# Optimization experiments

Measured on AMD Instinct MI355X. Metric: run time of the kernel, lower is better.

## Reference

```python
import jax, jax.numpy as jnp
import numpy as np
from jax import lax


def _conv3d(x, w, b, circular=False):
    # x: (B,C,D,H,W), w: (O,I,kd,kh,kw)
    if circular:
        x = jnp.pad(x, ((0, 0), (0, 0), (1, 1), (1, 1), (1, 1)), mode='wrap')
    y = lax.conv_general_dilated(x, w, (1, 1, 1), 'VALID',
                                 dimension_numbers=('NCDHW', 'OIDHW', 'NCDHW'))
    return y + b[None, :, None, None, None]


def _inorm(x):
    # InstanceNorm3d, affine=False, eps=1e-5, biased variance over spatial dims
    mu = jnp.mean(x, axis=(2, 3, 4), keepdims=True)
    var = jnp.var(x, axis=(2, 3, 4), keepdims=True)
    return (x - mu) * lax.rsqrt(var + 1e-5)


def _gelu(x):
    return jax.nn.gelu(x, approximate=False)


def _r6_to_matrix(r6):
    eps = 1e-7
    v1 = r6[..., :3]
    v1 = v1 / (jnp.linalg.norm(v1, axis=-1, keepdims=True) + eps)
    v2 = r6[..., 3:]
    v2 = v2 - jnp.sum(v2 * v1, -1, keepdims=True) * v1
    v2 = v2 / (jnp.linalg.norm(v2, axis=-1, keepdims=True) + eps)
    v3 = jnp.cross(v1, v2)
    det = jnp.linalg.det(jnp.stack([v1, v2, v3], axis=-2))
    v3 = jnp.where(det[..., None] < 0, -v3, v3)
    return jnp.stack([v1, v2, v3], axis=-2)


def _ensure_matrix(R):
    def fnorm(v):
        return v / jnp.maximum(jnp.linalg.norm(v, axis=-1, keepdims=True), 1e-12)
    v1 = fnorm(R[..., 0, :] + 1e-6)
    v2 = R[..., 1, :]
    v2 = fnorm(v2 - jnp.sum(v2 * v1, -1, keepdims=True) * v1 + 1e-6)
    v3 = jnp.cross(v1, v2)
    det = jnp.linalg.det(jnp.stack([v1, v2, v3], axis=-2))
    v3 = jnp.where(det[..., None] < 0, -v3, v3)
    Rn = jnp.stack([v1, v2, v3], axis=-2)
    Rt = jnp.swapaxes(Rn, -2, -1)
    return 0.5 * (Rn + Rt @ Rn @ Rt)


def _rotate(X, R):
    # X: (bd, nh, L, hd); R: (nh, 3, 3). Pads hd to a multiple of 3, rotates
    # each 3-vector group by R^T-on-the-right (X_rot = X @ R^T).
    hd = X.shape[-1]
    pad = (-hd) % 3
    Xp = jnp.pad(X, ((0, 0), (0, 0), (0, 0), (0, pad))) if pad else X
    nv = Xp.shape[-1] // 3
    Xr = Xp.reshape(Xp.shape[:-1] + (nv, 3))
    Y = jnp.einsum('bhlvi,hji->bhlvj', Xr, R).reshape(Xp.shape)
    return Y[..., :hd] if pad else Y


def _forward(x, pos_emb, qkv_w, qkv_b, lp_w1, lp_b1, lp_w2, lp_b2,
             mod_w1, mod_b1, mod_w2, mod_b2, pa_w, pa_b,
             proj_w, proj_b, pos_bias_w, pos_bias_b,
             A_d, A_h, A_w, R_d, R_h, R_w, t_d, t_h, t_w):
    B, C, D, H, W = x.shape
    nh = pa_w.shape[0]
    hd = C // nh
    scale = hd ** -0.5

    # PositionalProcessing (identical for all three axial passes)
    lf = _conv3d(pos_emb, lp_w1, lp_b1, circular=True)
    lf = _conv3d(_gelu(_inorm(lf)), lp_w2, lp_b2)
    m = _conv3d(lf, mod_w1, mod_b1)
    m = jax.nn.sigmoid(_conv3d(_gelu(_inorm(m)), mod_w2, mod_b2))
    x_mod = x * m                                   # (B,C,D,H,W)
    pa = _gelu(_inorm(_conv3d(pos_emb, pa_w, pa_b)))  # (B,nh,D,H,W)

    def axial(comp, perm, inv_perm, A, R, t):
        xp = jnp.transpose(x_mod, perm)             # (B, a, b, C, L)
        Bp, a, b, _, L = xp.shape
        bd = Bp * a * b
        xf = jnp.swapaxes(xp.reshape(bd, C, L), 1, 2)  # (bd, L, C)
        qkv = (xf @ qkv_w.T + qkv_b).reshape(bd, L, 3, nh, hd)
        qkv = jnp.transpose(qkv, (2, 0, 3, 1, 4))
        q, k, v = qkv[0], qkv[1], qkv[2]
        R_qk = _r6_to_matrix(A[0].astype(jnp.float32))  # (nh,3,3), same for all bd
        R_v = _ensure_matrix(R[0])                      # (nh,3,3)
        q_r, k_r, v_r = _rotate(q, R_qk), _rotate(k, R_qk), _rotate(v, R_v)
        # axis positions: linspace on one coordinate component
        pos = jnp.zeros((L, 3), x.dtype).at[:, comp].set(jnp.linspace(-1.0, 1.0, L))
        pos_t = pos[None] + t[0]                        # (nh, L, 3)
        rel = pos_t[:, :, None, :] - pos_t[:, None, :, :]  # (nh, L, L, 3)
        bias = jnp.einsum('hqkc,c->hqk', rel, pos_bias_w[0]) + pos_bias_b[0]
        pa_p = jnp.transpose(pa, perm).reshape(bd, nh, L)
        attn = jnp.einsum('bhqd,bhkd->bhqk', q_r, k_r) * scale
        attn = jax.nn.softmax(attn + pa_p[..., None] + bias[None], axis=-1)
        out = jnp.einsum('bhqk,bhkd->bhqd', attn, v_r)
        out = jnp.transpose(out, (0, 2, 1, 3)).reshape(Bp, a, b, L, C)
        return jnp.transpose(out, inv_perm)             # back to (B,C,D,H,W)

    out = (axial(2, (0, 3, 4, 1, 2), (0, 4, 3, 1, 2), A_d, R_d, t_d)
           + axial(1, (0, 2, 4, 1, 3), (0, 4, 1, 3, 2), A_h, R_h, t_h)
           + axial(0, (0, 2, 3, 1, 4), (0, 4, 1, 2, 3), A_w, R_w, t_w))
    return jnp.einsum('oc,bcdhw->bodhw', proj_w[:, :, 0, 0, 0], out) + proj_b[None, :, None, None, None]


def setup_inputs() -> dict:
    key = jax.random.key(0)
    B, C, D, H, W, nh = 2, 128, 32, 32, 32, 8
    ks = jax.random.split(key, 24)

    def n(k, shape, s=0.05):
        return (jax.random.normal(k, shape) * s).astype(jnp.float32)

    def r6(k):
        k1, k2 = jax.random.split(k)
        v1 = jax.random.normal(k1, (1, nh, 3))
        v1 = v1 / jnp.linalg.norm(v1, axis=-1, keepdims=True)
        v2 = jax.random.normal(k2, (1, nh, 3))
        v2 = v2 - jnp.sum(v2 * v1, -1, keepdims=True) * v1
        v2 = v2 / jnp.linalg.norm(v2, axis=-1, keepdims=True)
        return jnp.concatenate([v1, v2], -1).astype(jnp.float32)

    eye = jnp.broadcast_to(jnp.eye(3, dtype=jnp.float32), (1, nh, 3, 3))
    return {
        'x': jax.random.normal(ks[0], (B, C, D, H, W), jnp.float32),
        'pos_emb': jax.random.normal(ks[1], (B, C, D, H, W), jnp.float32),
        'qkv_w': n(ks[2], (3 * C, C)), 'qkv_b': n(ks[3], (3 * C,)),
        'lp_w1': n(ks[4], (C, C, 3, 3, 3), 0.02), 'lp_b1': n(ks[5], (C,)),
        'lp_w2': n(ks[6], (C, C, 1, 1, 1)), 'lp_b2': n(ks[7], (C,)),
        'mod_w1': n(ks[8], (C, C, 1, 1, 1)), 'mod_b1': n(ks[9], (C,)),
        'mod_w2': n(ks[10], (C, C, 1, 1, 1)), 'mod_b2': n(ks[11], (C,)),
        'pa_w': n(ks[12], (nh, C, 1, 1, 1)), 'pa_b': n(ks[13], (nh,)),
        'proj_w': n(ks[14], (C, C, 1, 1, 1)), 'proj_b': n(ks[15], (C,)),
        'pos_bias_w': n(ks[16], (1, 3), 0.5), 'pos_bias_b': n(ks[17], (1,)),
        'A_d': r6(ks[18]), 'A_h': r6(ks[19]), 'A_w': r6(ks[20]),
        'R_d': eye, 'R_h': eye, 'R_w': eye,
        't_d': n(ks[21], (1, nh, 1, 3), 0.01),
        't_h': n(ks[22], (1, nh, 1, 3), 0.01),
        't_w': n(ks[23], (1, nh, 1, 3), 0.01),
    }


def reference(x, pos_emb, qkv_w, qkv_b, lp_w1, lp_b1, lp_w2, lp_b2,
              mod_w1, mod_b1, mod_w2, mod_b2, pa_w, pa_b,
              proj_w, proj_b, pos_bias_w, pos_bias_b,
              A_d, A_h, A_w, R_d, R_h, R_w, t_d, t_h, t_w):
    return _forward(x, pos_emb, qkv_w, qkv_b, lp_w1, lp_b1, lp_w2, lp_b2,
                    mod_w1, mod_b1, mod_w2, mod_b2, pa_w, pa_b,
                    proj_w, proj_b, pos_bias_w, pos_bias_b,
                    A_d, A_h, A_w, R_d, R_h, R_w, t_d, t_h, t_w)
```

## Files before the change

### kernel.cpp

```cpp
#include <hip/hip_runtime.h>
#include <cstdint>
#include <cstddef>


#define NTOK 65536
#define SPAT 32768

#define WS_R0     0ull
#define WS_A0     0ull
#define WS_A1     4194304ull
#define WS_MPREB  8388608ull
#define WS_A2     8388608ull
#define WS_XTOKB  12582912ull
#define WS_INT    16777216ull
#define WS_QKVH   20971520ull
#define WS_CONVP  33554432ull
#define WS_QKVP   33775616ull
#define WS_WCP    33800192ull
#define WS_MODW2P 33808384ull
#define WS_PROJP  33816576ull
#define WS_BC     33824768ull
#define WS_RBUF   33824896ull
#define WS_PS     33825328ull
#define WS_PSS    33956400ull
#define WS_MU1    34087472ull
#define WS_RS1    34087728ull
#define WS_MU2    34087984ull
#define WS_RS2    34088240ull

typedef __attribute__((ext_vector_type(8))) short short8;
typedef __attribute__((ext_vector_type(4))) float f32x4;
typedef __attribute__((ext_vector_type(16))) float f32x16;

__device__ __forceinline__ float gelu_f(float x) {
  return 0.5f * x * (1.0f + erff(x * 0.70710678118654752f));
}
__device__ __forceinline__ float sigmoid_f(float x) {
  return 1.0f / (1.0f + expf(-x));
}
__device__ __forceinline__ unsigned short f2bf(float x) {
  unsigned int u = __float_as_uint(x);
  unsigned int r = u + 0x7fffu + ((u >> 16) & 1u);
  return (unsigned short)(r >> 16);
}
__device__ __forceinline__ float bf2f(unsigned short u) {
  return __uint_as_float(((unsigned int)u) << 16);
}
__device__ __forceinline__ void bf16x16_load(const unsigned short* p, float* f) {
  const uint4 a = *(const uint4*)p;
  const uint4 b = *(const uint4*)(p + 8);
  const unsigned int w[8] = {a.x, a.y, a.z, a.w, b.x, b.y, b.z, b.w};
  #pragma unroll
  for (int i = 0; i < 8; ++i) {
    f[2 * i] = __uint_as_float(w[i] << 16);
    f[2 * i + 1] = __uint_as_float(w[i] & 0xffff0000u);
  }
}
__device__ __forceinline__ void gload_lds16(const void* g, void* l) {
  __builtin_amdgcn_global_load_lds(
      (const __attribute__((address_space(1))) unsigned int*)g,
      (__attribute__((address_space(3))) unsigned int*)l, 16, 0, 0);
}
__device__ __forceinline__ float dot3(const float* a, const float* b) {
  return a[0] * b[0] + a[1] * b[1] + a[2] * b[2];
}
__device__ __forceinline__ void cross3(const float* a, const float* b, float* c) {
  c[0] = a[1] * b[2] - a[2] * b[1];
  c[1] = a[2] * b[0] - a[0] * b[2];
  c[2] = a[0] * b[1] - a[1] * b[0];
}

__device__ void r6_to_matrix(const float* r6, float* R) {
  float v1[3] = {r6[0], r6[1], r6[2]};
  float n1 = sqrtf(dot3(v1, v1));
  float inv1 = 1.0f / (n1 + 1e-7f);
  v1[0] *= inv1; v1[1] *= inv1; v1[2] *= inv1;
  float v2[3] = {r6[3], r6[4], r6[5]};
  float d = dot3(v2, v1);
  v2[0] -= d * v1[0]; v2[1] -= d * v1[1]; v2[2] -= d * v1[2];
  float n2 = sqrtf(dot3(v2, v2));
  float inv2 = 1.0f / (n2 + 1e-7f);
  v2[0] *= inv2; v2[1] *= inv2; v2[2] *= inv2;
  float v3[3]; cross3(v1, v2, v3);
  float cx[3]; cross3(v2, v3, cx);
  float det = dot3(v1, cx);
  if (det < 0.0f) { v3[0] = -v3[0]; v3[1] = -v3[1]; v3[2] = -v3[2]; }
  R[0] = v1[0]; R[1] = v1[1]; R[2] = v1[2];
  R[3] = v2[0]; R[4] = v2[1]; R[5] = v2[2];
  R[6] = v3[0]; R[7] = v3[1]; R[8] = v3[2];
}

__device__ void ensure_matrix(const float* Rin, float* Ro) {
  float a[3] = {Rin[0] + 1e-6f, Rin[1] + 1e-6f, Rin[2] + 1e-6f};
  float na = fmaxf(sqrtf(dot3(a, a)), 1e-12f);
  float v1[3] = {a[0] / na, a[1] / na, a[2] / na};
  float b0[3] = {Rin[3], Rin[4], Rin[5]};
  float d = dot3(b0, v1);
  float bb[3] = {b0[0] - d * v1[0] + 1e-6f, b0[1] - d * v1[1] + 1e-6f, b0[2] - d * v1[2] + 1e-6f};
  float nb = fmaxf(sqrtf(dot3(bb, bb)), 1e-12f);
  float v2[3] = {bb[0] / nb, bb[1] / nb, bb[2] / nb};
  float v3[3]; cross3(v1, v2, v3);
  float cx[3]; cross3(v2, v3, cx);
  float det = dot3(v1, cx);
  if (det < 0.0f) { v3[0] = -v3[0]; v3[1] = -v3[1]; v3[2] = -v3[2]; }
  float Rn[9] = {v1[0], v1[1], v1[2], v2[0], v2[1], v2[2], v3[0], v3[1], v3[2]};
  float T1[9], T2[9];
  for (int i = 0; i < 3; ++i)
    for (int j = 0; j < 3; ++j) {
      float s = 0.f;
      for (int k = 0; k < 3; ++k) s += Rn[k * 3 + i] * Rn[k * 3 + j];
      T1[i * 3 + j] = s;
    }
  for (int i = 0; i < 3; ++i)
    for (int j = 0; j < 3; ++j) {
      float s = 0.f;
      for (int k = 0; k < 3; ++k) s += T1[i * 3 + k] * Rn[j * 3 + k];
      T2[i * 3 + j] = s;
    }
  for (int i = 0; i < 9; ++i) Ro[i] = 0.5f * (Rn[i] + T2[i]);
}

__device__ __forceinline__ void rot16(const float* R, const float* x, float* y) {
  #pragma unroll
  for (int g = 0; g < 5; ++g) {
    float a = x[3 * g], b = x[3 * g + 1], c = x[3 * g + 2];
    y[3 * g + 0] = R[0] * a + R[1] * b + R[2] * c;
    y[3 * g + 1] = R[3] * a + R[4] * b + R[5] * c;
    y[3 * g + 2] = R[6] * a + R[7] * b + R[8] * c;
  }
  y[15] = R[0] * x[15];
}

__global__ __launch_bounds__(256) void prep_w_kernel(
    const float* __restrict__ lp_w1, const float* __restrict__ qkv_w,
    const float* __restrict__ mod_w1, const float* __restrict__ lp_w2,
    const float* __restrict__ lp_b2, const float* __restrict__ mod_b1,
    const float* __restrict__ mod_w2, const float* __restrict__ proj_w,
    const float* __restrict__ Ad, const float* __restrict__ Ah,
    const float* __restrict__ Aw, const float* __restrict__ Rd,
    const float* __restrict__ Rh, const float* __restrict__ Rw,
    unsigned short* __restrict__ convP, unsigned short* __restrict__ qkvP,
    unsigned short* __restrict__ WcP, unsigned short* __restrict__ modw2P,
    unsigned short* __restrict__ projP, float* __restrict__ bc,
    float* __restrict__ Rbuf) {
  int gid = blockIdx.x * 256 + threadIdx.x;
  for (int f = gid; f < 442368; f += 65536) {
    int e = f & 7;
    int co = (f >> 3) & 127;
    int rest = f >> 10;
    int l4 = rest & 3;
    int ks = (rest >> 2) & 3;
    int dxt = rest >> 4;
    int dx = dxt % 3;
    int tap = dxt / 3;
    int dz = tap / 3, dy = tap % 3;
    int ci = ks * 32 + l4 * 8 + e;
    convP[f] = f2bf(lp_w1[(co * 128 + ci) * 27 + dz * 9 + dy * 3 + dx]);
  }
  if (gid < 49152) qkvP[gid] = f2bf(qkv_w[gid]);
  if (gid < 16384) {
    modw2P[gid] = f2bf(mod_w2[gid]);
    projP[gid] = f2bf(proj_w[gid]);
    int o = gid >> 7, i = gid & 127;
    float s = 0.f;
    for (int c = 0; c < 128; ++c) s += mod_w1[o * 128 + c] * lp_w2[c * 128 + i];
    WcP[gid] = f2bf(s);
  }
  if (gid < 128) {
    float s = 0.f;
    for (int c = 0; c < 128; ++c) s += mod_w1[gid * 128 + c] * lp_b2[c];
    bc[gid] = s + mod_b1[gid];
  }
  if (blockIdx.x == 0 && threadIdx.x >= 224 && threadIdx.x < 248) {
    int tid = threadIdx.x - 224;
    int ax = tid >> 3, h = tid & 7;
    const float* A = (ax == 0) ? Ad : ((ax == 1) ? Ah : Aw);
    const float* R = (ax == 0) ? Rd : ((ax == 1) ? Rh : Rw);
    float Rq[9], Rv[9];
    r6_to_matrix(A + h * 6, Rq);
    ensure_matrix(R + h * 9, Rv);
    float* dst = Rbuf + (ax * 8 + h) * 18;
    for (int i = 0; i < 9; ++i) { dst[i] = Rq[i]; dst[9 + i] = Rv[i]; }
  }
}

__global__ __launch_bounds__(256) void transpose_kernel(const float* __restrict__ x,
                                                        const float* __restrict__ pe,
                                                        unsigned short* __restrict__ xtokb,
                                                        unsigned short* __restrict__ inT) {
  __shared__ float lds[32][132];
  int blk = blockIdx.x;
  int b = blk >> 10;
  int dh = blk & 1023;
  int tid = threadIdx.x;
  size_t planebase = ((size_t)b << 22) + ((size_t)dh << 5);
  size_t tb = ((size_t)blk) << 5;
  #pragma unroll
  for (int r = 0; r < 16; ++r) {
    int idx = r * 256 + tid;
    int ci = idx >> 5, w = idx & 31;
    lds[w][ci] = x[planebase + ((size_t)ci << 15) + w];
  }
  __syncthreads();
  #pragma unroll
  for (int r = 0; r < 16; ++r) {
    int idx = r * 256 + tid;
    int w = idx >> 7, ci = idx & 127;
    xtokb[(tb + w) * 128 + ci] = f2bf(lds[w][ci]);
  }
  __syncthreads();
  #pragma unroll
  for (int r = 0; r < 16; ++r) {
    int idx = r * 256 + tid;
    int ci = idx >> 5, w = idx & 31;
    lds[w][ci] = pe[planebase + ((size_t)ci << 15) + w];
  }
  __syncthreads();
  #pragma unroll
  for (int r = 0; r < 16; ++r) {
    int idx = r * 256 + tid;
    int w = idx >> 7, ci = idx & 127;
    inT[(tb + w) * 128 + ci] = f2bf(lds[w][ci]);
  }
}

__global__ __launch_bounds__(256, 4) void conv_mfma_kernel(
    const unsigned short* __restrict__ inT, const unsigned short* __restrict__ Bp,
    const float* __restrict__ b1, unsigned short* __restrict__ out,
    float* __restrict__ ps, float* __restrict__ pss) {
  __shared__ unsigned short Als[16384];
  __shared__ float sumb[128];
  __shared__ float sqb[128];
  const int blk = blockIdx.x;
  const int b = blk >> 9, d = (blk >> 4) & 31, hg = blk & 15;
  const int h0 = hg << 1;
  const int tid = threadIdx.x;
  const int lane = tid & 63;
  const int wid = tid >> 6;
  const int l15 = lane & 15, l4 = lane >> 4;

  f32x4 acc[4][2];
  #pragma unroll
  for (int mt = 0; mt < 4; ++mt)
    #pragma unroll
    for (int nt = 0; nt < 2; ++nt)
      #pragma unroll
      for (int r = 0; r < 4; ++r) acc[mt][nt][r] = 0.f;

  int mw[4], mhh[4];
  #pragma unroll
  for (int mt = 0; mt < 4; ++mt) {
    int m = mt * 16 + l15;
    mhh[mt] = m >> 5;
    mw[mt] = m & 31;
  }
  const size_t tokbase = ((size_t)b << 15) + ((size_t)d << 10) + ((size_t)h0 << 5);

  auto stage = [&](int dz) {
    const int zr = (d + dz + 31) & 31;
    #pragma unroll
    for (int p = 0; p < 8; ++p) {
      const int g = p * 256 + tid;
      const int tok = g >> 4, gi = g & 15;
      const int r = tok >> 5, w = tok & 31;
      const int yr = (h0 + r + 31) & 31;
      const size_t srcbyte = ((((size_t)b << 15) + ((size_t)zr << 10) + ((size_t)yr << 5) + w) << 8)
                             + (size_t)((gi ^ (w & 7)) << 4);
      gload_lds16((const char*)inT + srcbyte, (char*)Als + (size_t)g * 16);
    }
  };

  auto compute = [&](int dz) {
    #pragma unroll
    for (int dy = 0; dy < 3; ++dy) {
      const int tap = dz * 3 + dy;
      #pragma unroll
      for (int dx = 0; dx < 3; ++dx) {
        int abase[4], asw[4];
        #pragma unroll
        for (int mt = 0; mt < 4; ++mt) {
          const int wsft = (mw[mt] + dx + 31) & 31;
          const int stok = (mhh[mt] + dy) * 32 + wsft;
          abase[mt] = stok * 256;
          asw[mt] = (wsft & 7) << 4;
        }
        #pragma unroll
        for (int ks = 0; ks < 4; ++ks) {
          const int k2 = (ks * 32 + l4 * 8) * 2;
          const int bbase = (((tap * 3 + dx) * 4 + ks) * 4 + l4) * 1024;
          short8 afr[4], bfr[2];
          #pragma unroll
          for (int nt = 0; nt < 2; ++nt) {
            const int co = wid * 32 + nt * 16 + l15;
            bfr[nt] = *(const short8*)(Bp + bbase + co * 8);
          }
          #pragma unroll
          for (int mt = 0; mt < 4; ++mt)
            afr[mt] = *(const short8*)((const char*)Als + abase[mt] + (k2 ^ asw[mt]));
          __builtin_amdgcn_s_setprio(1);
          #pragma unroll
          for (int mt = 0; mt < 4; ++mt)
            #pragma unroll
            for (int nt = 0; nt < 2; ++nt)
              acc[mt][nt] = __builtin_amdgcn_mfma_f32_16x16x32_bf16(afr[mt], bfr[nt],
                                                                    acc[mt][nt], 0, 0, 0);
          __builtin_amdgcn_s_setprio(0);
        }
      }
    }
  };

  for (int dz = 0; dz < 3; ++dz) {
    stage(dz);
    __syncthreads();
    compute(dz);
    if (dz < 2) __syncthreads();
  }

  #pragma unroll
  for (int nt = 0; nt < 2; ++nt) {
    const int co = wid * 32 + nt * 16 + l15;
    const float bias = b1[co];
    float s = 0.f, q = 0.f;
    #pragma unroll
    for (int mt = 0; mt < 4; ++mt) {
      #pragma unroll
      for (int r = 0; r < 4; ++r) {
        const int m = mt * 16 + l4 * 4 + r;
        const float v = acc[mt][nt][r] + bias;
        out[(tokbase + m) * 128 + co] = f2bf(v);
        s += v; q += v * v;
      }
    }
    s += __shfl_xor(s, 16); s += __shfl_xor(s, 32);
    q += __shfl_xor(q, 16); q += __shfl_xor(q, 32);
    if (l4 == 0) { sumb[co] = s; sqb[co] = q; }
  }
  __syncthreads();
  if (tid < 128) {
    ps[blk * 128 + tid] = sumb[tid];
    pss[blk * 128 + tid] = sqb[tid];
  }
}

__global__ __launch_bounds__(64) void stats_final_kernel(
    const float* __restrict__ ps, const float* __restrict__ pss,
    float* __restrict__ mu, float* __restrict__ rs, int nb) {
  const int pair = blockIdx.x;
  const int b = pair >> 7, c = pair & 127;
  const int lane = threadIdx.x;
  float s = 0.f, ss = 0.f;
  for (int j = lane; j < nb; j += 64) {
    const int idx = ((b * nb + j) << 7) + c;
    s += ps[idx];
    ss += pss[idx];
  }
  #pragma unroll
  for (int o = 32; o > 0; o >>= 1) {
    s += __shfl_xor(s, o);
    ss += __shfl_xor(ss, o);
  }
  if (lane == 0) {
    float m = s * (1.0f / 32768.0f);
    float v = ss * (1.0f / 32768.0f) - m * m;
    mu[pair] = m;
    rs[pair] = rsqrtf(v + 1e-5f);
  }
}

template <int PRE, int AB16, int POST, int STATS>
__global__ __launch_bounds__(256) void gemm_mfma_kernel(
    const void* __restrict__ Avoid, const unsigned short* __restrict__ Wp,
    const float* __restrict__ bias, void* __restrict__ Yvoid, int O,
    const float* __restrict__ mu, const float* __restrict__ rs,
    const unsigned short* __restrict__ xtb, float* __restrict__ ps,
    float* __restrict__ pss) {
  __shared__ float sumb[128][2];
  __shared__ float sqb[128][2];
  const int tid = threadIdx.x;
  const int lane = tid & 63, wid = tid >> 6;
  const int wm = wid >> 1, wn = wid & 1;
  const int l15 = lane & 15, l4 = lane >> 4;
  const int og = blockIdx.x * 128;
  const int t0 = blockIdx.y * 128;
  const int bidx = t0 >> 15;
  const float* Af = (const float*)Avoid;
  const unsigned short* Ab = (const unsigned short*)Avoid;
  float* Yf = (float*)Yvoid;
  unsigned short* Yb = (unsigned short*)Yvoid;

  f32x4 acc[4][4];
  #pragma unroll
  for (int mt = 0; mt < 4; ++mt)
    #pragma unroll
    for (int nt = 0; nt < 4; ++nt)
      #pragma unroll
      for (int r = 0; r < 4; ++r) acc[mt][nt][r] = 0.f;

  #pragma unroll
  for (int ks = 0; ks < 4; ++ks) {
    const int kb = ks * 32 + l4 * 8;
    short8 a[4], bfr[4];
    float4 m0, m1, r0, r1;
    if constexpr (PRE == 1) {
      m0 = *(const float4*)(mu + bidx * 128 + kb);
      m1 = *(const float4*)(mu + bidx * 128 + kb + 4);
      r0 = *(const float4*)(rs + bidx * 128 + kb);
      r1 = *(const float4*)(rs + bidx * 128 + kb + 4);
    }
    #pragma unroll
    for (int mt = 0; mt < 4; ++mt) {
      const int tok = t0 + wm * 64 + mt * 16 + l15;
      float v[16];
      bool have = false;
      if constexpr (AB16 == 1) {
        if constexpr (PRE == 1) {
          bf16x16_load(Ab + (size_t)tok * 128 + kb, v);
          have = true;
        } else {
          a[mt] = *(const short8*)(Ab + (size_t)tok * 128 + kb);
        }
      } else {
        const float* ap = Af + (size_t)tok * 128 + kb;
        float4 v0 = *(const float4*)ap;
        float4 v1 = *(const float4*)(ap + 4);
        v[0] = v0.x; v[1] = v0.y; v[2] = v0.z; v[3] = v0.w;
        v[4] = v1.x; v[5] = v1.y; v[6] = v1.z; v[7] = v1.w;
        have = true;
      }
      if (have) {
        if constexpr (PRE == 1) {
          const float mm[8] = {m0.x, m0.y, m0.z, m0.w, m1.x, m1.y, m1.z, m1.w};
          const float rr[8] = {r0.x, r0.y, r0.z, r0.w, r1.x, r1.y, r1.z, r1.w};
          #pragma unroll
          for (int j = 0; j < 8; ++j) v[j] = gelu_f((v[j] - mm[j]) * rr[j]);
        }
        short8 t;
        #pragma unroll
        for (int j = 0; j < 8; ++j) t[j] = (short)f2bf(v[j]);
        a[mt] = t;
      }
    }
    #pragma unroll
    for (int nt = 0; nt < 4; ++nt) {
      const int o = og + wn * 64 + nt * 16 + l15;
      bfr[nt] = *(const short8*)(Wp + (size_t)o * 128 + kb);
    }
    #pragma unroll
    for (int mt = 0; mt < 4; ++mt)
      #pragma unroll
      for (int nt = 0; nt < 4; ++nt)
        acc[mt][nt] = __builtin_amdgcn_mfma_f32_16x16x32_bf16(a[mt], bfr[nt], acc[mt][nt], 0, 0, 0);
  }

  #pragma unroll
  for (int nt = 0; nt < 4; ++nt) {
    const int o = og + wn * 64 + nt * 16 + l15;
    const float bb = bias[o];
    float s = 0.f, q = 0.f;
    #pragma unroll
    for (int mt = 0; mt < 4; ++mt) {
      #pragma unroll
      for (int r = 0; r < 4; ++r) {
        const int t = t0 + wm * 64 + mt * 16 + l4 * 4 + r;
        const float v = acc[mt][nt][r] + bb;
        if constexpr (POST == 0) {
          Yf[(size_t)t * O + o] = v;
        } else if constexpr (POST == 1) {
          Yb[(size_t)t * 128 + o] = f2bf(sigmoid_f(v) * bf2f(xtb[(size_t)t * 128 + o]));
        } else if constexpr (POST == 2) {
          Yb[(size_t)t * O + o] = f2bf(v);
        } else {
          const int sec = o >> 7, hsub = (o & 127) >> 4, ch = o & 15;
          Yb[(size_t)t * 384 + hsub * 48 + sec * 16 + ch] = f2bf(v);
        }
        if constexpr (STATS) { s += v; q += v * v; }
      }
    }
    if constexpr (STATS) {
      s += __shfl_xor(s, 16); s += __shfl_xor(s, 32);
      q += __shfl_xor(q, 16); q += __shfl_xor(q, 32);
      if (l4 == 0) { sumb[o - og][wm] = s; sqb[o - og][wm] = q; }
    }
  }
  if constexpr (STATS) {
    __syncthreads();
    if (tid < 128) {
      ps[blockIdx.y * 128 + tid] = sumb[tid][0] + sumb[tid][1];
      pss[blockIdx.y * 128 + tid] = sqb[tid][0] + sqb[tid][1];
    }
  }
}

__global__ __launch_bounds__(256) void proj_mfma_kernel(
    const unsigned short* __restrict__ A0b, const unsigned short* __restrict__ A1b,
    const unsigned short* __restrict__ A2b, const unsigned short* __restrict__ Wp,
    const float* __restrict__ bias, float* __restrict__ out) {
  const int tid = threadIdx.x;
  const int lane = tid & 63, wid = tid >> 6;
  const int wm = wid >> 1, wn = wid & 1;
  const int l15 = lane & 15, l4 = lane >> 4;
  const int t0 = blockIdx.x * 128;

  f32x4 acc[4][4];
  #pragma unroll
  for (int mt = 0; mt < 4; ++mt)
    #pragma unroll
    for (int nt = 0; nt < 4; ++nt)
      #pragma unroll
      for (int r = 0; r < 4; ++r) acc[mt][nt][r] = 0.f;

  #pragma unroll
  for (int ks = 0; ks < 4; ++ks) {
    const int kb = ks * 32 + l4 * 8;
    short8 a[4], bfr[4];
    #pragma unroll
    for (int mt = 0; mt < 4; ++mt) {
      const int o = wm * 64 + mt * 16 + l15;
      a[mt] = *(const short8*)(Wp + (size_t)o * 128 + kb);
    }
    #pragma unroll
    for (int nt = 0; nt < 4; ++nt) {
      const int tok = t0 + wn * 64 + nt * 16 + l15;
      const size_t off = (size_t)tok * 128 + kb;
      short8 s0 = *(const short8*)(A0b + off);
      short8 s1 = *(const short8*)(A1b + off);
      short8 s2 = *(const short8*)(A2b + off);
      short8 r;
      #pragma unroll
      for (int i = 0; i < 8; ++i) {
        float f = bf2f((unsigned short)s0[i]) + bf2f((unsigned short)s1[i]) +
                  bf2f((unsigned short)s2[i]);
        r[i] = (short)f2bf(f);
      }
      bfr[nt] = r;
    }
    #pragma unroll
    for (int mt = 0; mt < 4; ++mt)
      #pragma unroll
      for (int nt = 0; nt < 4; ++nt)
        acc[mt][nt] = __builtin_amdgcn_mfma_f32_16x16x32_bf16(a[mt], bfr[nt], acc[mt][nt], 0, 0, 0);
  }

  #pragma unroll
  for (int nt = 0; nt < 4; ++nt) {
    const int tok = t0 + wn * 64 + nt * 16 + l15;
    const int dhw = tok & 32767, bB = tok >> 15;
    #pragma unroll
    for (int mt = 0; mt < 4; ++mt) {
      #pragma unroll
      for (int r = 0; r < 4; ++r) {
        const int o = wm * 64 + mt * 16 + l4 * 4 + r;
        out[((size_t)(bB * 128 + o) << 15) + dhw] = acc[mt][nt][r] + bias[o];
      }
    }
  }
}

__global__ __launch_bounds__(512) void attn_mfma_kernel(
    const unsigned short* __restrict__ qkvt, const float* __restrict__ Rbuf,
    const float* __restrict__ pbw, unsigned short* __restrict__ a0,
    unsigned short* __restrict__ a1, unsigned short* __restrict__ a2) {
  __shared__ unsigned short rows[32 * 392];
  __shared__ unsigned short Vt[8][16 * 40];
  __shared__ float Ot[8][32 * 20];
  const int axial = blockIdx.y;
  const int seq = blockIdx.x;
  unsigned short* dstbuf = (axial == 0) ? a0 : ((axial == 1) ? a1 : a2);
  const int tid = threadIdx.x;
  const int lane = tid & 63, head = tid >> 6;
  const int tok = lane & 31, hi = lane >> 5;
  const int b = seq >> 10, rem = seq & 1023;
  const int u = rem >> 5, v = rem & 31;
  int base, stride, comp;
  if (axial == 0)      { base = (b << 15) + (u << 5) + v;         stride = 1024; comp = 2; }
  else if (axial == 1) { base = (b << 15) + (u << 10) + v;        stride = 32;   comp = 1; }
  else                 { base = (b << 15) + (u << 10) + (v << 5); stride = 1;    comp = 0; }

  #pragma unroll
  for (int p = 0; p < 3; ++p) {
    const int c = p * 512 + tid;
    const int r = c / 48, cw = c - r * 48;
    const size_t src = ((size_t)base + (size_t)r * stride) * 384 + (size_t)cw * 8;
    *(uint4*)((char*)rows + r * 784 + cw * 16) = *(const uint4*)(qkvt + src);
  }
  __syncthreads();

  const float* Rp = Rbuf + (axial * 8 + head) * 18;
  const float rq00 = fabsf(Rp[0]);
  const unsigned short* myrow = rows + tok * 392 + head * 48;
  short8 aq = *(const short8*)(myrow + hi * 8);
  short8 ak = *(const short8*)(myrow + 16 + hi * 8);
  short8 av = *(const short8*)(myrow + 32 + hi * 8);
  if (hi) {
    aq[7] = (short)f2bf(bf2f((unsigned short)aq[7]) * rq00);
    ak[7] = (short)f2bf(bf2f((unsigned short)ak[7]) * rq00);
  }
  #pragma unroll
  for (int e = 0; e < 8; ++e) Vt[head][(hi * 8 + e) * 40 + tok] = (unsigned short)av[e];

  f32x16 sacc;
  #pragma unroll
  for (int r = 0; r < 16; ++r) sacc[r] = 0.f;
  sacc = __builtin_amdgcn_mfma_f32_32x32x16_bf16(ak, aq, sacc, 0, 0, 0);
  const float wb = pbw[comp];
  float p[16];
  float mmax = -1e30f;
  #pragma unroll
  for (int r = 0; r < 16; ++r) {
    const int kk = (r & 3) + 4 * hi + 8 * (r >> 2);
    const float lin = -1.0f + (2.0f / 31.0f) * (float)kk;
    p[r] = sacc[r] * 0.25f - lin * wb;
    mmax = fmaxf(mmax, p[r]);
  }
  mmax = fmaxf(mmax, __shfl_xor(mmax, 32));
  float sum = 0.f;
  #pragma unroll
  for (int r = 0; r < 16; ++r) { p[r] = expf(p[r] - mmax); sum += p[r]; }
  sum += __shfl_xor(sum, 32);
  const float inv = 1.0f / sum;
  #pragma unroll
  for (int r = 0; r < 16; ++r) p[r] *= inv;
  unsigned pk[8], sw[8];
  #pragma unroll
  for (int j = 0; j < 8; ++j) {
    unsigned r_;
    asm("v_cvt_pk_bf16_f32 %0, %1, %2" : "=v"(r_) : "v"(p[2 * j]), "v"(p[2 * j + 1]));
    pk[j] = r_;
  }
  #pragma unroll
  for (int j = 0; j < 8; ++j) sw[j] = (unsigned)__shfl_xor((int)pk[j], 32);
  uint4 Fu, Gu;
  Fu.x = hi ? sw[2] : pk[0];
  Fu.y = hi ? sw[3] : pk[1];
  Fu.z = hi ? pk[2] : sw[0];
  Fu.w = hi ? pk[3] : sw[1];
  Gu.x = hi ? sw[6] : pk[4];
  Gu.y = hi ? sw[7] : pk[5];
  Gu.z = hi ? pk[6] : sw[4];
  Gu.w = hi ? pk[7] : sw[5];
  short8 Pf = *(short8*)&Fu;
  short8 Pg = *(short8*)&Gu;
  const unsigned short* vrow = Vt[head] + (tok & 15) * 40;
  short8 Bv0 = *(const short8*)(vrow + hi * 8);
  short8 Bv1 = *(const short8*)(vrow + 16 + hi * 8);
  f32x16 oacc;
  #pragma unroll
  for (int r = 0; r < 16; ++r) oacc[r] = 0.f;
  oacc = __builtin_amdgcn_mfma_f32_32x32x16_bf16(Pf, Bv0, oacc, 0, 0, 0);
  oacc = __builtin_amdgcn_mfma_f32_32x32x16_bf16(Pg, Bv1, oacc, 0, 0, 0);
  if (tok < 16) {
    #pragma unroll
    for (int r = 0; r < 16; ++r) {
      const int q = (r & 3) + 4 * hi + 8 * (r >> 2);
      Ot[head][q * 20 + tok] = oacc[r];
    }
  }
  if (lane < 32) {
    float o16[16], y16[16], Rv[9];
    #pragma unroll
    for (int j = 0; j < 16; ++j) o16[j] = Ot[head][lane * 20 + j];
    #pragma unroll
    for (int i = 0; i < 9; ++i) Rv[i] = Rp[9 + i];
    rot16(Rv, o16, y16);
    unsigned outw[8];
    #pragma unroll
    for (int j = 0; j < 8; ++j)
      outw[j] = ((unsigned)f2bf(y16[2 * j + 1]) << 16) | (unsigned)f2bf(y16[2 * j]);
    const size_t t2 = (size_t)base + (size_t)lane * stride;
    unsigned short* dst = dstbuf + t2 * 128 + head * 16;
    uint4 o0 = {outw[0], outw[1], outw[2], outw[3]};
    uint4 o1 = {outw[4], outw[5], outw[6], outw[7]};
    *(uint4*)dst = o0;
    *(uint4*)(dst + 8) = o1;
  }
}

extern "C" void kernel_launch(void* const* d_in, const int* in_sizes, int n_in,
                              void* d_out, int out_size, void* d_ws, size_t ws_size,
                              hipStream_t stream) {
  const float* x       = (const float*)d_in[0];
  const float* pos_emb = (const float*)d_in[1];
  const float* qkv_w   = (const float*)d_in[2];
  const float* qkv_b   = (const float*)d_in[3];
  const float* lp_w1   = (const float*)d_in[4];
  const float* lp_b1   = (const float*)d_in[5];
  const float* lp_w2   = (const float*)d_in[6];
  const float* lp_b2   = (const float*)d_in[7];
  const float* mod_w1  = (const float*)d_in[8];
  const float* mod_b1  = (const float*)d_in[9];
  const float* mod_w2  = (const float*)d_in[10];
  const float* mod_b2  = (const float*)d_in[11];
  const float* proj_w  = (const float*)d_in[14];
  const float* proj_b  = (const float*)d_in[15];
  const float* pbw     = (const float*)d_in[16];
  const float* Ad      = (const float*)d_in[18];
  const float* Ah      = (const float*)d_in[19];
  const float* Aw      = (const float*)d_in[20];
  const float* Rd      = (const float*)d_in[21];
  const float* Rh      = (const float*)d_in[22];
  const float* Rw      = (const float*)d_in[23];

  float* ws = (float*)d_ws;
  unsigned short* lfb    = (unsigned short*)(ws + WS_R0);
  unsigned short* A0b    = (unsigned short*)(ws + WS_A0);
  unsigned short* A1b    = (unsigned short*)(ws + WS_A1);
  unsigned short* A2b    = (unsigned short*)(ws + WS_A2);
  unsigned short* mpreb  = (unsigned short*)(ws + WS_MPREB);
  unsigned short* xtokb  = (unsigned short*)(ws + WS_XTOKB);
  unsigned short* inT    = (unsigned short*)(ws + WS_INT);
  unsigned short* qkvt   = (unsigned short*)(ws + WS_QKVH);
  unsigned short* convP  = (unsigned short*)(ws + WS_CONVP);
  unsigned short* qkvP   = (unsigned short*)(ws + WS_QKVP);
  unsigned short* WcP    = (unsigned short*)(ws + WS_WCP);
  unsigned short* modw2P = (unsigned short*)(ws + WS_MODW2P);
  unsigned short* projP  = (unsigned short*)(ws + WS_PROJP);
  float* bc     = ws + WS_BC;
  float* Rbuf   = ws + WS_RBUF;
  float* ps     = ws + WS_PS;
  float* pss    = ws + WS_PSS;
  float* mu1    = ws + WS_MU1;
  float* rs1    = ws + WS_RS1;
  float* mu2    = ws + WS_MU2;
  float* rs2    = ws + WS_RS2;
  unsigned short* xmodb = inT;

  prep_w_kernel<<<256, 256, 0, stream>>>(lp_w1, qkv_w, mod_w1, lp_w2, lp_b2, mod_b1,
                                         mod_w2, proj_w, Ad, Ah, Aw, Rd, Rh, Rw,
                                         convP, qkvP, WcP, modw2P, projP, bc, Rbuf);
  transpose_kernel<<<2048, 256, 0, stream>>>(x, pos_emb, xtokb, inT);
  conv_mfma_kernel<<<1024, 256, 0, stream>>>(inT, convP, lp_b1, lfb, ps, pss);
  stats_final_kernel<<<256, 64, 0, stream>>>(ps, pss, mu1, rs1, 512);
  gemm_mfma_kernel<1, 1, 2, 1><<<dim3(1, 512), 256, 0, stream>>>(
      lfb, WcP, bc, mpreb, 128, mu1, rs1, nullptr, ps, pss);
  stats_final_kernel<<<256, 64, 0, stream>>>(ps, pss, mu2, rs2, 256);
  gemm_mfma_kernel<1, 1, 1, 0><<<dim3(1, 512), 256, 0, stream>>>(
      mpreb, modw2P, mod_b2, xmodb, 128, mu2, rs2, xtokb, nullptr, nullptr);
  gemm_mfma_kernel<0, 1, 3, 0><<<dim3(3, 512), 256, 0, stream>>>(
      xmodb, qkvP, qkv_b, qkvt, 384, nullptr, nullptr, nullptr, nullptr, nullptr);
  attn_mfma_kernel<<<dim3(2048, 3), 512, 0, stream>>>(qkvt, Rbuf, pbw, A0b, A1b, A2b);
  proj_mfma_kernel<<<512, 256, 0, stream>>>(A0b, A1b, A2b, projP, proj_b, (float*)d_out);
}
```

Baseline: 274.1 us.

## Fuse gating GEMM with QKV GEMM via LDS, merge prep and transpose kernels

Adds a gateqkv kernel that runs the mod_w2 GEMM with the norm+GELU prologue and sigmoid gating, keeps the gated 128x128 tile in swizzled LDS, then computes all three QKV output chunks from it. This removes the global round trip of the gated activations and one launch. Weight prep and the input transpose become one launch, and conv block indices are remapped to change scheduling order. The cost is higher register and LDS use in the fused kernel and serial QKV chunks inside each block.

```diff
diff --git a/kernel.cpp b/kernel.cpp
--- a/kernel.cpp
+++ b/kernel.cpp
@@ -131,7 +131,7 @@
   y[15] = R[0] * x[15];
 }
 
-__global__ __launch_bounds__(256) void prep_w_kernel(
+__global__ __launch_bounds__(256) void prep_transpose_kernel(
     const float* __restrict__ lp_w1, const float* __restrict__ qkv_w,
     const float* __restrict__ mod_w1, const float* __restrict__ lp_w2,
     const float* __restrict__ lp_b2, const float* __restrict__ mod_b1,
@@ -139,57 +139,56 @@
     const float* __restrict__ Ad, const float* __restrict__ Ah,
     const float* __restrict__ Aw, const float* __restrict__ Rd,
     const float* __restrict__ Rh, const float* __restrict__ Rw,
+    const float* __restrict__ x, const float* __restrict__ pe,
     unsigned short* __restrict__ convP, unsigned short* __restrict__ qkvP,
     unsigned short* __restrict__ WcP, unsigned short* __restrict__ modw2P,
     unsigned short* __restrict__ projP, float* __restrict__ bc,
-    float* __restrict__ Rbuf) {
-  int gid = blockIdx.x * 256 + threadIdx.x;
-  for (int f = gid; f < 442368; f += 65536) {
-    int e = f & 7;
-    int co = (f >> 3) & 127;
-    int rest = f >> 10;
-    int l4 = rest & 3;
-    int ks = (rest >> 2) & 3;
-    int dxt = rest >> 4;
-    int dx = dxt % 3;
-    int tap = dxt / 3;
-    int dz = tap / 3, dy = tap % 3;
-    int ci = ks * 32 + l4 * 8 + e;
-    convP[f] = f2bf(lp_w1[(co * 128 + ci) * 27 + dz * 9 + dy * 3 + dx]);
-  }
-  if (gid < 49152) qkvP[gid] = f2bf(qkv_w[gid]);
-  if (gid < 16384) {
-    modw2P[gid] = f2bf(mod_w2[gid]);
-    projP[gid] = f2bf(proj_w[gid]);
-    int o = gid >> 7, i = gid & 127;
-    float s = 0.f;
-    for (int c = 0; c < 128; ++c) s += mod_w1[o * 128 + c] * lp_w2[c * 128 + i];
-    WcP[gid] = f2bf(s);
-  }
-  if (gid < 128) {
-    float s = 0.f;
-    for (int c = 0; c < 128; ++c) s += mod_w1[gid * 128 + c] * lp_b2[c];
-    bc[gid] = s + mod_b1[gid];
-  }
-  if (blockIdx.x == 0 && threadIdx.x >= 224 && threadIdx.x < 248) {
-    int tid = threadIdx.x - 224;
-    int ax = tid >> 3, h = tid & 7;
-    const float* A = (ax == 0) ? Ad : ((ax == 1) ? Ah : Aw);
-    const float* R = (ax == 0) ? Rd : ((ax == 1) ? Rh : Rw);
-    float Rq[9], Rv[9];
-    r6_to_matrix(A + h * 6, Rq);
-    ensure_matrix(R + h * 9, Rv);
-    float* dst = Rbuf + (ax * 8 + h) * 18;
-    for (int i = 0; i < 9; ++i) { dst[i] = Rq[i]; dst[9 + i] = Rv[i]; }
-  }
-}
-
-__global__ __launch_bounds__(256) void transpose_kernel(const float* __restrict__ x,
-                                                        const float* __restrict__ pe,
-                                                        unsigned short* __restrict__ xtokb,
-                                                        unsigned short* __restrict__ inT) {
+    float* __restrict__ Rbuf, unsigned short* __restrict__ xtokb,
+    unsigned short* __restrict__ inT) {
   __shared__ float lds[32][132];
-  int blk = blockIdx.x;
+  if (blockIdx.x < 256) {
+    int gid = blockIdx.x * 256 + threadIdx.x;
+    for (int f = gid; f < 442368; f += 65536) {
+      int e = f & 7;
+      int co = (f >> 3) & 127;
+      int rest = f >> 10;
+      int l4 = rest & 3;
+      int ks = (rest >> 2) & 3;
+      int dxt = rest >> 4;
+      int dx = dxt % 3;
+      int tap = dxt / 3;
+      int dz = tap / 3, dy = tap % 3;
+      int ci = ks * 32 + l4 * 8 + e;
+      convP[f] = f2bf(lp_w1[(co * 128 + ci) * 27 + dz * 9 + dy * 3 + dx]);
+    }
+    if (gid < 49152) qkvP[gid] = f2bf(qkv_w[gid]);
+    if (gid < 16384) {
+      modw2P[gid] = f2bf(mod_w2[gid]);
+      projP[gid] = f2bf(proj_w[gid]);
+      int o = gid >> 7, i = gid & 127;
+      float s = 0.f;
+      for (int c = 0; c < 128; ++c) s += mod_w1[o * 128 + c] * lp_w2[c * 128 + i];
+      WcP[gid] = f2bf(s);
+    }
+    if (gid < 128) {
+      float s = 0.f;
+      for (int c = 0; c < 128; ++c) s += mod_w1[gid * 128 + c] * lp_b2[c];
+      bc[gid] = s + mod_b1[gid];
+    }
+    if (blockIdx.x == 0 && threadIdx.x >= 224 && threadIdx.x < 248) {
+      int tid = threadIdx.x - 224;
+      int ax = tid >> 3, h = tid & 7;
+      const float* A = (ax == 0) ? Ad : ((ax == 1) ? Ah : Aw);
+      const float* R = (ax == 0) ? Rd : ((ax == 1) ? Rh : Rw);
+      float Rq[9], Rv[9];
+      r6_to_matrix(A + h * 6, Rq);
+      ensure_matrix(R + h * 9, Rv);
+      float* dst = Rbuf + (ax * 8 + h) * 18;
+      for (int i = 0; i < 9; ++i) { dst[i] = Rq[i]; dst[9 + i] = Rv[i]; }
+    }
+    return;
+  }
+  int blk = blockIdx.x - 256;
   int b = blk >> 10;
   int dh = blk & 1023;
   int tid = threadIdx.x;
@@ -231,7 +230,8 @@
   __shared__ unsigned short Als[16384];
   __shared__ float sumb[128];
   __shared__ float sqb[128];
-  const int blk = blockIdx.x;
+  const int orig = blockIdx.x;
+  const int blk = ((orig & 7) << 7) + (orig >> 3);
   const int b = blk >> 9, d = (blk >> 4) & 31, hg = blk & 15;
   const int h0 = hg << 1;
   const int tid = threadIdx.x;
@@ -466,13 +466,8 @@
         const float v = acc[mt][nt][r] + bb;
         if constexpr (POST == 0) {
           Yf[(size_t)t * O + o] = v;
-        } else if constexpr (POST == 1) {
-          Yb[(size_t)t * 128 + o] = f2bf(sigmoid_f(v) * bf2f(xtb[(size_t)t * 128 + o]));
         } else if constexpr (POST == 2) {
           Yb[(size_t)t * O + o] = f2bf(v);
-        } else {
-          const int sec = o >> 7, hsub = (o & 127) >> 4, ch = o & 15;
-          Yb[(size_t)t * 384 + hsub * 48 + sec * 16 + ch] = f2bf(v);
         }
         if constexpr (STATS) { s += v; q += v * v; }
       }
@@ -488,6 +483,120 @@
     if (tid < 128) {
       ps[blockIdx.y * 128 + tid] = sumb[tid][0] + sumb[tid][1];
       pss[blockIdx.y * 128 + tid] = sqb[tid][0] + sqb[tid][1];
+    }
+  }
+}
+
+__global__ __launch_bounds__(256) void gateqkv_mfma_kernel(
+    const unsigned short* __restrict__ mpreb, const unsigned short* __restrict__ modw2P,
+    const float* __restrict__ mod_b2, const unsigned short* __restrict__ xtb,
+    const unsigned short* __restrict__ qkvP, const float* __restrict__ qkv_b,
+    unsigned short* __restrict__ qkvt, const float* __restrict__ mu,
+    const float* __restrict__ rs) {
+  __shared__ char xm[32768];
+  const int tid = threadIdx.x;
+  const int lane = tid & 63, wid = tid >> 6;
+  const int wm = wid >> 1, wn = wid & 1;
+  const int l15 = lane & 15, l4 = lane >> 4;
+  const int t0 = blockIdx.x * 128;
+  const int bidx = t0 >> 15;
+
+  f32x4 acc[4][4];
+  #pragma unroll
+  for (int mt = 0; mt < 4; ++mt)
+    #pragma unroll
+    for (int nt = 0; nt < 4; ++nt)
+      #pragma unroll
+      for (int r = 0; r < 4; ++r) acc[mt][nt][r] = 0.f;
+
+  #pragma unroll
+  for (int ks = 0; ks < 4; ++ks) {
+    const int kb = ks * 32 + l4 * 8;
+    short8 a[4], bfr[4];
+    const float4 m0 = *(const float4*)(mu + bidx * 128 + kb);
+    const float4 m1 = *(const float4*)(mu + bidx * 128 + kb + 4);
+    const float4 r0 = *(const float4*)(rs + bidx * 128 + kb);
+    const float4 r1 = *(const float4*)(rs + bidx * 128 + kb + 4);
+    const float mm[8] = {m0.x, m0.y, m0.z, m0.w, m1.x, m1.y, m1.z, m1.w};
+    const float rr[8] = {r0.x, r0.y, r0.z, r0.w, r1.x, r1.y, r1.z, r1.w};
+    #pragma unroll
+    for (int mt = 0; mt < 4; ++mt) {
+      const int tok = t0 + wm * 64 + mt * 16 + l15;
+      float v[16];
+      bf16x16_load(mpreb + (size_t)tok * 128 + kb, v);
+      short8 t;
+      #pragma unroll
+      for (int j = 0; j < 8; ++j) t[j] = (short)f2bf(gelu_f((v[j] - mm[j]) * rr[j]));
+      a[mt] = t;
+    }
+    #pragma unroll
+    for (int nt = 0; nt < 4; ++nt) {
+      const int o = wn * 64 + nt * 16 + l15;
+      bfr[nt] = *(const short8*)(modw2P + (size_t)o * 128 + kb);
+    }
+    #pragma unroll
+    for (int mt = 0; mt < 4; ++mt)
+      #pragma unroll
+      for (int nt = 0; nt < 4; ++nt)
+        acc[mt][nt] = __builtin_amdgcn_mfma_f32_16x16x32_bf16(a[mt], bfr[nt], acc[mt][nt], 0, 0, 0);
+  }
+  #pragma unroll
+  for (int nt = 0; nt < 4; ++nt) {
+    const int o = wn * 64 + nt * 16 + l15;
+    const float bb = mod_b2[o];
+    #pragma unroll
+    for (int mt = 0; mt < 4; ++mt) {
+      #pragma unroll
+      for (int r = 0; r < 4; ++r) {
+        const int tl = wm * 64 + mt * 16 + l4 * 4 + r;
+        const int t = t0 + tl;
+        const float v = sigmoid_f(acc[mt][nt][r] + bb) * bf2f(xtb[(size_t)t * 128 + o]);
+        *(unsigned short*)(xm + tl * 256 + ((o * 2) ^ ((tl & 7) << 4))) = f2bf(v);
+      }
+    }
+  }
+  __syncthreads();
+
+  for (int c = 0; c < 3; ++c) {
+    #pragma unroll
+    for (int mt = 0; mt < 4; ++mt)
+      #pragma unroll
+      for (int nt = 0; nt < 4; ++nt)
+        #pragma unroll
+        for (int r = 0; r < 4; ++r) acc[mt][nt][r] = 0.f;
+    #pragma unroll
+    for (int ks = 0; ks < 4; ++ks) {
+      const int kb = ks * 32 + l4 * 8;
+      short8 a[4], bfr[4];
+      #pragma unroll
+      for (int mt = 0; mt < 4; ++mt) {
+        const int tl = wm * 64 + mt * 16 + l15;
+        a[mt] = *(const short8*)(xm + tl * 256 + ((kb * 2) ^ ((tl & 7) << 4)));
+      }
+      #pragma unroll
+      for (int nt = 0; nt < 4; ++nt) {
+        const int o = c * 128 + wn * 64 + nt * 16 + l15;
+        bfr[nt] = *(const short8*)(qkvP + (size_t)o * 128 + kb);
+      }
+      #pragma unroll
+      for (int mt = 0; mt < 4; ++mt)
+        #pragma unroll
+        for (int nt = 0; nt < 4; ++nt)
+          acc[mt][nt] = __builtin_amdgcn_mfma_f32_16x16x32_bf16(a[mt], bfr[nt], acc[mt][nt], 0, 0, 0);
+    }
+    #pragma unroll
+    for (int nt = 0; nt < 4; ++nt) {
+      const int o = c * 128 + wn * 64 + nt * 16 + l15;
+      const float bb = qkv_b[o];
+      const int hsub = (o & 127) >> 4, ch = o & 15;
+      #pragma unroll
+      for (int mt = 0; mt < 4; ++mt) {
+        #pragma unroll
+        for (int r = 0; r < 4; ++r) {
+          const int t = t0 + wm * 64 + mt * 16 + l4 * 4 + r;
+          qkvt[(size_t)t * 384 + hsub * 48 + c * 16 + ch] = f2bf(acc[mt][nt][r] + bb);
+        }
+      }
     }
   }
 }
@@ -723,21 +832,18 @@
   float* rs1    = ws + WS_RS1;
   float* mu2    = ws + WS_MU2;
   float* rs2    = ws + WS_RS2;
-  unsigned short* xmodb = inT;
-
-  prep_w_kernel<<<256, 256, 0, stream>>>(lp_w1, qkv_w, mod_w1, lp_w2, lp_b2, mod_b1,
-                                         mod_w2, proj_w, Ad, Ah, Aw, Rd, Rh, Rw,
-                                         convP, qkvP, WcP, modw2P, projP, bc, Rbuf);
-  transpose_kernel<<<2048, 256, 0, stream>>>(x, pos_emb, xtokb, inT);
+
+  prep_transpose_kernel<<<2304, 256, 0, stream>>>(
+      lp_w1, qkv_w, mod_w1, lp_w2, lp_b2, mod_b1, mod_w2, proj_w,
+      Ad, Ah, Aw, Rd, Rh, Rw, x, pos_emb,
+      convP, qkvP, WcP, modw2P, projP, bc, Rbuf, xtokb, inT);
   conv_mfma_kernel<<<1024, 256, 0, stream>>>(inT, convP, lp_b1, lfb, ps, pss);
   stats_final_kernel<<<256, 64, 0, stream>>>(ps, pss, mu1, rs1, 512);
   gemm_mfma_kernel<1, 1, 2, 1><<<dim3(1, 512), 256, 0, stream>>>(
       lfb, WcP, bc, mpreb, 128, mu1, rs1, nullptr, ps, pss);
   stats_final_kernel<<<256, 64, 0, stream>>>(ps, pss, mu2, rs2, 256);
-  gemm_mfma_kernel<1, 1, 1, 0><<<dim3(1, 512), 256, 0, stream>>>(
-      mpreb, modw2P, mod_b2, xmodb, 128, mu2, rs2, xtokb, nullptr, nullptr);
-  gemm_mfma_kernel<0, 1, 3, 0><<<dim3(3, 512), 256, 0, stream>>>(
-      xmodb, qkvP, qkv_b, qkvt, 384, nullptr, nullptr, nullptr, nullptr, nullptr);
+  gateqkv_mfma_kernel<<<512, 256, 0, stream>>>(
+      mpreb, modw2P, mod_b2, xtokb, qkvP, qkv_b, qkvt, mu2, rs2);
   attn_mfma_kernel<<<dim3(2048, 3), 512, 0, stream>>>(qkvt, Rbuf, pbw, A0b, A1b, A2b);
   proj_mfma_kernel<<<512, 256, 0, stream>>>(A0b, A1b, A2b, projP, proj_b, (float*)d_out);
 }
```

Result: faster. 251.0 us (-8.5%).
